# Performance work log

Measured on AMD Instinct MI355X. Metric: run time of the kernel, lower is better.

The kernel has to match this reference:

```python
import jax, jax.numpy as jnp
import numpy as np

B, C, T, D = 4, 248, 500, 64


def setup_inputs() -> dict:
    key = jax.random.key(0)
    ks = jax.random.split(key, 7)
    scale = 1.0  # nn.Linear(1, d) default init is U(-1, 1); exact dist irrelevant for correctness baseline
    return {
        "x": jax.random.normal(ks[0], (B, C, T), dtype=jnp.float32),
        "wq": jax.random.uniform(ks[1], (D,), jnp.float32, -scale, scale),
        "bq": jax.random.uniform(ks[2], (D,), jnp.float32, -scale, scale),
        "wk": jax.random.uniform(ks[3], (D,), jnp.float32, -scale, scale),
        "bk": jax.random.uniform(ks[4], (D,), jnp.float32, -scale, scale),
        "wv": jax.random.uniform(ks[5], (D,), jnp.float32, -scale, scale),
        "bv": jax.random.uniform(ks[6], (D,), jnp.float32, -scale, scale),
    }


def reference(x, wq, bq, wk, bk, wv, bv):
    # x: [B, C, T] -> xt: [B, T, C]; each scalar projected to attn_dim D
    xt = jnp.transpose(x, (0, 2, 1))
    Q = xt[..., None] * wq + bq            # [B, T, C, D]
    K = xt[..., None] * wk + bk            # [B, T, C, D]
    V = xt[..., None] * wv + bv            # [B, T, C, D]
    d = Q.shape[-1]
    # channel-wise attention per (B, T) slice
    scores = jnp.einsum("btcd,bted->btce", Q, K) / jnp.sqrt(jnp.float32(d))
    wts = jax.nn.softmax(scores, axis=-1)  # [B, T, C, C] (dropout=0 / eval mode)
    out = jnp.einsum("btce,bted->btcd", wts, V).mean(axis=2)  # [B, T, D]
    return out, wts
```

## Files before the change

### kernel.cpp

```cpp
#include <hip/hip_runtime.h>
#include <math.h>

#define BB 4
#define CC 248
#define TT 500
#define DD 64

typedef float f32x4 __attribute__((ext_vector_type(4)));

__global__ __launch_bounds__(256) void csa_kernel(
    const float* __restrict__ x,
    const float* __restrict__ wq, const float* __restrict__ bq,
    const float* __restrict__ wk, const float* __restrict__ bk,
    const float* __restrict__ wv, const float* __restrict__ bv,
    float* __restrict__ out, float* __restrict__ wts)
{
    const int bt = blockIdx.x;
    const int b  = bt / TT;
    const int t  = bt % TT;
    const int tid  = threadIdx.x;
    const int wave = tid >> 6;
    const int lane = tid & 63;
    const int q    = lane & 31;
    const int h    = lane >> 5;

    __shared__ __align__(16) float xs[CC];
    __shared__ float sred[8];
    __shared__ float sA, sB2, sXmax, sXmin, sYbar;

    if (tid < CC) xs[tid] = x[((size_t)b * CC + tid) * TT + t];

    if (wave == 1) {
        float wkv = wk[lane];
        float pa = wq[lane] * wkv;
        float pb = bq[lane] * wkv;
        #pragma unroll
        for (int off = 32; off > 0; off >>= 1) {
            pa += __shfl_xor(pa, off, 64);
            pb += __shfl_xor(pb, off, 64);
        }
        if (lane == 0) { sA = pa * 0.125f; sB2 = pb * 0.125f; }
    }
    __syncthreads();

    float vmax = -INFINITY, vmin = INFINITY;
    if (tid < CC) { vmax = xs[tid]; vmin = vmax; }
    #pragma unroll
    for (int off = 32; off > 0; off >>= 1) {
        vmax = fmaxf(vmax, __shfl_xor(vmax, off, 64));
        vmin = fminf(vmin, __shfl_xor(vmin, off, 64));
    }
    if (lane == 0) { sred[wave] = vmax; sred[4 + wave] = vmin; }
    __syncthreads();
    if (tid == 0) {
        sXmax = fmaxf(fmaxf(sred[0], sred[1]), fmaxf(sred[2], sred[3]));
        sXmin = fminf(fminf(sred[4], sred[5]), fminf(sred[6], sred[7]));
    }
    __syncthreads();

    const float LOG2E = 1.4426950408889634f;
    const float a2   = sA  * LOG2E;
    const float b22  = sB2 * LOG2E;
    const float xmax = sXmax;
    const float xmin = sXmin;

    const f32x4* xs4 = reinterpret_cast<const f32x4*>(xs);
    const bool act = (q < 31);
    f32x4 xlo = {0.f,0.f,0.f,0.f}, xhi = {0.f,0.f,0.f,0.f};
    if (act) { xlo = xs4[q]; xhi = xs4[31 + q]; }

    float ysum = 0.f;
    const size_t slice = (size_t)bt * (CC * CC);

    #pragma unroll 2
    for (int i = 0; i < 31; ++i) {
        const int r = 8 * i + 2 * wave + h;
        const float scl = fmaf(a2, xs[r], b22);
        const float ml  = (scl >= 0.f) ? scl * xmax : scl * xmin;

        f32x4 plo = {0.f,0.f,0.f,0.f}, phi = {0.f,0.f,0.f,0.f};
        float sum = 0.f, xp = 0.f;
        if (act) {
            plo.x = __builtin_amdgcn_exp2f(fmaf(scl, xlo.x, -ml));
            plo.y = __builtin_amdgcn_exp2f(fmaf(scl, xlo.y, -ml));
            plo.z = __builtin_amdgcn_exp2f(fmaf(scl, xlo.z, -ml));
            plo.w = __builtin_amdgcn_exp2f(fmaf(scl, xlo.w, -ml));
            phi.x = __builtin_amdgcn_exp2f(fmaf(scl, xhi.x, -ml));
            phi.y = __builtin_amdgcn_exp2f(fmaf(scl, xhi.y, -ml));
            phi.z = __builtin_amdgcn_exp2f(fmaf(scl, xhi.z, -ml));
            phi.w = __builtin_amdgcn_exp2f(fmaf(scl, xhi.w, -ml));
            sum = ((plo.x + plo.y) + (plo.z + plo.w)) + ((phi.x + phi.y) + (phi.z + phi.w));
            xp  = ((plo.x * xlo.x + plo.y * xlo.y) + (plo.z * xlo.z + plo.w * xlo.w))
                + ((phi.x * xhi.x + phi.y * xhi.y) + (phi.z * xhi.z + phi.w * xhi.w));
        }
        #pragma unroll
        for (int off = 16; off > 0; off >>= 1) {
            sum += __shfl_xor(sum, off, 64);
            xp  += __shfl_xor(xp,  off, 64);
        }
        const float inv = __builtin_amdgcn_rcpf(sum);

        if (act) {
            f32x4 olo, ohi;
            olo.x = plo.x * inv; olo.y = plo.y * inv; olo.z = plo.z * inv; olo.w = plo.w * inv;
            ohi.x = phi.x * inv; ohi.y = phi.y * inv; ohi.z = phi.z * inv; ohi.w = phi.w * inv;
            f32x4* dst = reinterpret_cast<f32x4*>(wts + slice + (size_t)r * CC);
            dst[q]      = olo;
            dst[31 + q] = ohi;
        }
        ysum += xp * inv;
    }

    if (q == 0) sred[wave * 2 + h] = ysum;
    __syncthreads();
    if (tid == 0) {
        float s = 0.f;
        #pragma unroll
        for (int k = 0; k < 8; ++k) s += sred[k];
        sYbar = s * (1.0f / CC);
    }
    __syncthreads();

    if (tid < DD)
        out[(size_t)bt * DD + tid] = fmaf(wv[tid], sYbar, bv[tid]);
}

extern "C" void kernel_launch(void* const* d_in, const int* in_sizes, int n_in,
                              void* d_out, int out_size, void* d_ws, size_t ws_size,
                              hipStream_t stream) {
    const float* x  = (const float*)d_in[0];
    const float* wq = (const float*)d_in[1];
    const float* bq = (const float*)d_in[2];
    const float* wk = (const float*)d_in[3];
    const float* bk = (const float*)d_in[4];
    const float* wv = (const float*)d_in[5];
    const float* bv = (const float*)d_in[6];

    float* out = (float*)d_out;
    float* wts = (float*)d_out + (size_t)BB * TT * DD;

    csa_kernel<<<dim3(BB * TT), dim3(256), 0, stream>>>(x, wq, bq, wk, bk, wv, bv, out, wts);
}
```

Baseline: 104.5 us.

## Split softmax into stats pass and separate full-wave recompute-and-store pass

```diff
diff --git a/kernel.cpp b/kernel.cpp
--- a/kernel.cpp
+++ b/kernel.cpp
@@ -25,6 +25,7 @@
     const int h    = lane >> 5;
 
     __shared__ __align__(16) float xs[CC];
+    __shared__ __align__(16) float sRow[CC][4];
     __shared__ float sred[8];
     __shared__ float sA, sB2, sXmax, sXmin, sYbar;
 
@@ -65,12 +66,11 @@
     const float xmin = sXmin;
 
     const f32x4* xs4 = reinterpret_cast<const f32x4*>(xs);
-    const bool act = (q < 31);
+    const bool act31 = (q < 31);
     f32x4 xlo = {0.f,0.f,0.f,0.f}, xhi = {0.f,0.f,0.f,0.f};
-    if (act) { xlo = xs4[q]; xhi = xs4[31 + q]; }
+    if (act31) { xlo = xs4[q]; xhi = xs4[31 + q]; }
 
     float ysum = 0.f;
-    const size_t slice = (size_t)bt * (CC * CC);
 
     #pragma unroll 2
     for (int i = 0; i < 31; ++i) {
@@ -78,9 +78,9 @@
         const float scl = fmaf(a2, xs[r], b22);
         const float ml  = (scl >= 0.f) ? scl * xmax : scl * xmin;
 
-        f32x4 plo = {0.f,0.f,0.f,0.f}, phi = {0.f,0.f,0.f,0.f};
         float sum = 0.f, xp = 0.f;
-        if (act) {
+        if (act31) {
+            f32x4 plo, phi;
             plo.x = __builtin_amdgcn_exp2f(fmaf(scl, xlo.x, -ml));
             plo.y = __builtin_amdgcn_exp2f(fmaf(scl, xlo.y, -ml));
             plo.z = __builtin_amdgcn_exp2f(fmaf(scl, xlo.z, -ml));
@@ -99,16 +99,13 @@
             xp  += __shfl_xor(xp,  off, 64);
         }
         const float inv = __builtin_amdgcn_rcpf(sum);
+        ysum += xp * inv;
 
-        if (act) {
-            f32x4 olo, ohi;
-            olo.x = plo.x * inv; olo.y = plo.y * inv; olo.z = plo.z * inv; olo.w = plo.w * inv;
-            ohi.x = phi.x * inv; ohi.y = phi.y * inv; ohi.z = phi.z * inv; ohi.w = phi.w * inv;
-            f32x4* dst = reinterpret_cast<f32x4*>(wts + slice + (size_t)r * CC);
-            dst[q]      = olo;
-            dst[31 + q] = ohi;
+        if (q == 0) {
+            sRow[r][0] = scl;
+            sRow[r][1] = -ml;
+            sRow[r][2] = inv;
         }
-        ysum += xp * inv;
     }
 
     if (q == 0) sred[wave * 2 + h] = ysum;
@@ -119,7 +116,27 @@
         for (int k = 0; k < 8; ++k) s += sred[k];
         sYbar = s * (1.0f / CC);
     }
+
+    const bool act62 = (lane < 62);
+    f32x4 xv = {0.f,0.f,0.f,0.f};
     __syncthreads();
+    if (act62) xv = xs4[lane];
+
+    const size_t slice = (size_t)bt * (CC * CC);
+    const int rbase = wave * 62;
+    float* wbase = wts + slice + (size_t)rbase * CC;
+
+    #pragma unroll 4
+    for (int j = 0; j < 62; ++j) {
+        const f32x4 prm = *reinterpret_cast<const f32x4*>(sRow[rbase + j]);
+        f32x4 o;
+        o.x = __builtin_amdgcn_exp2f(fmaf(prm.x, xv.x, prm.y)) * prm.z;
+        o.y = __builtin_amdgcn_exp2f(fmaf(prm.x, xv.y, prm.y)) * prm.z;
+        o.z = __builtin_amdgcn_exp2f(fmaf(prm.x, xv.z, prm.y)) * prm.z;
+        o.w = __builtin_amdgcn_exp2f(fmaf(prm.x, xv.w, prm.y)) * prm.z;
+        if (act62)
+            reinterpret_cast<f32x4*>(wbase + (size_t)j * CC)[lane] = o;
+    }
 
     if (tid < DD)
         out[(size_t)bt * DD + tid] = fmaf(wv[tid], sYbar, bv[tid]);
```

Measured after the change: 112.9 us. 8.0% more time.
